# Kernel optimization log

Measured on AMD Instinct MI355X. Metric: run time of the kernel, lower is better.

## Reference

```python
import jax, jax.numpy as jnp
import numpy as np

B, T, H, O = 256, 512, 1024, 256


def setup_inputs() -> dict:
    key = jax.random.key(0)
    k0, k1, k2, k3, k4 = jax.random.split(key, 5)
    scale_ih = 1.0 / np.sqrt(1 + H)
    scale_ho = 1.0 / np.sqrt(H)
    return {
        "x": jax.random.normal(k0, (B, T), dtype=jnp.float32),
        "W_ih": jax.random.normal(k1, (1 + H, H), dtype=jnp.float32) * scale_ih,
        "b_ih": jax.random.normal(k2, (H,), dtype=jnp.float32) * scale_ih,
        "W_ho": jax.random.normal(k3, (H, O), dtype=jnp.float32) * scale_ho,
        "b_ho": jax.random.normal(k4, (O,), dtype=jnp.float32) * scale_ho,
    }


def reference(x, W_ih, b_ih, W_ho, b_ho):
    # Elman RNN cell: hidden = tanh(W_ih @ [x_t; h]); output = W_ho @ h_T.
    # Only the final timestep's output is returned by the original module,
    # so h2o is applied once to the final hidden state (identical math).
    batch = x.shape[0]
    h0 = jnp.zeros((batch, W_ih.shape[1]), dtype=x.dtype)

    def step(h, x_t):  # x_t: [B], h: [B, H]
        combined = jnp.concatenate([x_t[:, None], h], axis=1)  # [B, 1+H]
        h_new = jnp.tanh(combined @ W_ih + b_ih)               # [B, H]
        return h_new, None

    h_final, _ = jax.lax.scan(step, h0, x.T)  # scan over T
    return h_final @ W_ho + b_ho              # [B, O]
```

## Files before the change

kernel.cpp:

```cpp
#include <hip/hip_runtime.h>
#include <hip/hip_bf16.h>


#define Bsz 256
#define Tn  512
#define Hn  1024
#define On  256

typedef __attribute__((ext_vector_type(8))) _Float16 f16x8;
typedef __attribute__((ext_vector_type(4))) float f32x4;
typedef __attribute__((ext_vector_type(4))) int   i32x4;
typedef __attribute__((ext_vector_type(2))) int   i32x2;

__device__ __forceinline__ unsigned f2h(float f) {
    _Float16 h = (_Float16)f;
    union { _Float16 h; unsigned short s; } u; u.h = h;
    return (unsigned)u.s;
}

__device__ __forceinline__ f16x8 as_f16x8(i32x4 v) {
    union { i32x4 i; f16x8 h; } u; u.i = v; return u.h;
}

__device__ __forceinline__ float fast_tanh(float x) {
    float xc = fminf(fmaxf(x, -9.f), 9.f);
    float e  = __builtin_amdgcn_exp2f(xc * 2.8853900817779268f);
    return (e - 1.f) * __builtin_amdgcn_rcpf(e + 1.f);
}

#define MFMA_F16 __builtin_amdgcn_mfma_f32_16x16x32_f16

__device__ __forceinline__ void stage_quarter(const short* __restrict__ hsrc,
                                              short* __restrict__ htile,
                                              int row0, int cg, int kq,
                                              int lane, unsigned tag) {
    const int half = lane >> 5, gl = lane & 31, r0 = cg * 8;
    const short* a0 = hsrc + (size_t)(row0 + r0 + half) * Hn + kq * 256 + gl * 8;
    const short* a1 = a0 + 2 * Hn;
    const short* a2 = a0 + 4 * Hn;
    const short* a3 = a0 + 6 * Hn;
    i32x4 t0, t1, t2, t3;
    for (;;) {
        asm volatile(
            "global_load_dwordx4 %0, %4, off sc0 sc1\n\t"
            "global_load_dwordx4 %1, %5, off sc0 sc1\n\t"
            "global_load_dwordx4 %2, %6, off sc0 sc1\n\t"
            "global_load_dwordx4 %3, %7, off sc0 sc1\n\t"
            "s_waitcnt vmcnt(0)"
            : "=&v"(t0), "=&v"(t1), "=&v"(t2), "=&v"(t3)
            : "v"(a0), "v"(a1), "v"(a2), "v"(a3) : "memory");
        unsigned bad = 0;
#pragma unroll
        for (int e = 0; e < 4; ++e)
            bad |= (unsigned)(t0[e] ^ tag) | (unsigned)(t1[e] ^ tag) |
                   (unsigned)(t2[e] ^ tag) | (unsigned)(t3[e] ^ tag);
        if (!__any(bad & 1u)) break;
        unsigned p0, p3;
        do {
            asm volatile(
                "global_load_dword %0, %2, off sc0 sc1\n\t"
                "global_load_dword %1, %3, off sc0 sc1\n\t"
                "s_waitcnt vmcnt(0)"
                : "=&v"(p0), "=&v"(p3)
                : "v"(a0), "v"(a3) : "memory");
        } while (__any(((p0 ^ tag) | (p3 ^ tag)) & 1u));
    }
    i32x4 tv[4] = {t0, t1, t2, t3};
#pragma unroll
    for (int p = 0; p < 4; ++p) {
        int row = r0 + 2 * p + half;
        int g   = kq * 32 + gl;
        int idx = row * 128 + (g ^ (row & 7));
        *(i32x4*)(htile + idx * 8) = tv[p];
    }
}

__global__ __launch_bounds__(512, 2) void rnn_kernel(
    const float* __restrict__ x,
    const float* __restrict__ W_ih,
    const float* __restrict__ b_ih,
    const float* __restrict__ W_ho,
    const float* __restrict__ b_ho,
    float* __restrict__ out,
    short* __restrict__ hbuf)
{
    const int tid  = threadIdx.x;
    const int lane = tid & 63;
    const int w    = tid >> 6;
    const int cg   = w >> 2;
    const int kq   = w & 3;
    const int q    = lane >> 4;
    const int n    = lane & 15;

    const int i = blockIdx.x & 15;
    const int j = blockIdx.x >> 4;
    const int colbase = j * 128 + cg * 64;
    const int owncol  = colbase + kq * 16 + 4 * q;
    const int row0    = i * 16;

    __shared__ float x_lds[16][Tn + 1];
    __shared__ short htile[16 * Hn];
    __shared__ float redbuf[2][8 * 3 * 256];
    __shared__ int   pairflag[4];

    if (tid < 4) pairflag[tid] = 0;

    for (int idx = tid; idx < 16 * Tn; idx += 512) {
        int r = idx >> 9, tt = idx & (Tn - 1);
        x_lds[r][tt] = x[(row0 + r) * Tn + tt];
    }

    f16x8 wfrag[32];
#pragma unroll
    for (int mt = 0; mt < 4; ++mt)
#pragma unroll
        for (int ks = 0; ks < 8; ++ks) {
#pragma unroll
            for (int e = 0; e < 8; ++e) {
                int k = kq * 256 + ks * 32 + q * 8 + e;
                wfrag[mt * 8 + ks][e] =
                    (_Float16)W_ih[(size_t)(1 + k) * Hn + colbase + mt * 16 + n];
            }
        }
    const float4 bias4 = *(const float4*)(b_ih + owncol);
    const float4 w04   = *(const float4*)(W_ih + owncol);

    __syncthreads();

    short* h0 = hbuf;
    short* h1 = hbuf + Bsz * Hn;
    const int swn   = n & 7;
    const int gbase = kq * 32;
    const int slot  = (q * 16 + n) * 4;
    const f32x4 zero4 = {0.f, 0.f, 0.f, 0.f};

    for (int t = 0; t < Tn; ++t) {
        const float xv = x_lds[n][t];
        f32x4 aown = {bias4.x + xv * w04.x, bias4.y + xv * w04.y,
                      bias4.z + xv * w04.z, bias4.w + xv * w04.w};
        f32x4 hv;

        if (t > 0) {
            stage_quarter((t & 1) ? h1 : h0, htile, row0, cg, kq, lane,
                          (unsigned)((t + 1) >> 1) & 1u);
            asm volatile("s_waitcnt lgkmcnt(0)" ::: "memory");
            if (lane == 0)
                __hip_atomic_fetch_add(&pairflag[kq], 1, __ATOMIC_RELAXED,
                                       __HIP_MEMORY_SCOPE_WORKGROUP);
            while (__hip_atomic_load(&pairflag[kq], __ATOMIC_RELAXED,
                                     __HIP_MEMORY_SCOPE_WORKGROUP) < 2 * t) {}
            asm volatile("" ::: "memory");

            f32x4 acc0 = (kq == 0) ? aown : zero4;
            f32x4 acc1 = (kq == 1) ? aown : zero4;
            f32x4 acc2 = (kq == 2) ? aown : zero4;
            f32x4 acc3 = (kq == 3) ? aown : zero4;
            const i32x4* lrow = (const i32x4*)(htile + n * Hn);
#pragma unroll
            for (int ks = 0; ks < 8; ++ks) {
                f16x8 b = as_f16x8(lrow[(gbase + ks * 4 + q) ^ swn]);
                acc0 = MFMA_F16(wfrag[0 * 8 + ks], b, acc0, 0, 0, 0);
                acc1 = MFMA_F16(wfrag[1 * 8 + ks], b, acc1, 0, 0, 0);
                acc2 = MFMA_F16(wfrag[2 * 8 + ks], b, acc2, 0, 0, 0);
                acc3 = MFMA_F16(wfrag[3 * 8 + ks], b, acc3, 0, 0, 0);
            }

            float* rb = redbuf[t & 1];
#define WRITE_PART(MT, ACC)                                                  \
            if (kq != MT) {                                                  \
                int src = (kq < MT) ? kq : kq - 1;                           \
                *(f32x4*)(rb + ((cg * 4 + MT) * 3 + src) * 256 + slot) = ACC;\
            }
            WRITE_PART(0, acc0)
            WRITE_PART(1, acc1)
            WRITE_PART(2, acc2)
            WRITE_PART(3, acc3)
#undef WRITE_PART
            __syncthreads();

            hv = (kq == 0) ? acc0 : (kq == 1) ? acc1 : (kq == 2) ? acc2 : acc3;
            const float* bp = rb + (cg * 4 + kq) * 3 * 256 + slot;
            f32x4 p0 = *(const f32x4*)(bp);
            f32x4 p1 = *(const f32x4*)(bp + 256);
            f32x4 p2 = *(const f32x4*)(bp + 512);
            hv = hv + p0 + p1 + p2;
        } else {
            hv = aown;
        }

        unsigned tagn = (unsigned)((t + 2) >> 1) & 1u;
        unsigned e0 = f2h(fast_tanh(hv[0])), e1 = f2h(fast_tanh(hv[1]));
        unsigned e2 = f2h(fast_tanh(hv[2])), e3 = f2h(fast_tanh(hv[3]));
        i32x2 pk;
        pk[0] = (int)(((e0 & ~1u) | tagn) | (e1 << 16));
        pk[1] = (int)(((e2 & ~1u) | tagn) | (e3 << 16));
        short* hdst = (((t + 1) & 1) ? h1 : h0) + (size_t)(row0 + n) * Hn + owncol;
        asm volatile("global_store_dwordx2 %0, %1, off sc0 sc1"
                     :: "v"(hdst), "v"(pk) : "memory");
    }

    stage_quarter(h0, htile, row0, cg, kq, lane, 0u);
    __syncthreads();

    f32x4 e0 = zero4, e1 = zero4;
    {
        const i32x4* lrow = (const i32x4*)(htile + n * Hn);
#pragma unroll
        for (int kk = 0; kk < 4; ++kk) {
            f16x8 af = as_f16x8(lrow[(w * 16 + kk * 4 + q) ^ swn]);
            f16x8 b0, b1;
#pragma unroll
            for (int e = 0; e < 8; ++e) {
                const float* wp = W_ho +
                    (size_t)(w * 128 + kk * 32 + q * 8 + e) * On + j * 32 + n;
                b0[e] = (_Float16)wp[0];
                b1[e] = (_Float16)wp[16];
            }
            e0 = MFMA_F16(af, b0, e0, 0, 0, 0);
            e1 = MFMA_F16(af, b1, e1, 0, 0, 0);
        }
    }
    {
        float* re = redbuf[0] + w * 528;
#pragma unroll
        for (int r = 0; r < 4; ++r) {
            re[(4 * q + r) * 33 + n]      = e0[r];
            re[(4 * q + r) * 33 + 16 + n] = e1[r];
        }
    }
    __syncthreads();
    {
        int r = tid >> 5, c = tid & 31;
        float s = b_ho[j * 32 + c];
#pragma unroll
        for (int w8 = 0; w8 < 8; ++w8)
            s += redbuf[0][w8 * 528 + r * 33 + c];
        out[(size_t)(row0 + r) * On + j * 32 + c] = s;
    }
}

extern "C" void kernel_launch(void* const* d_in, const int* in_sizes, int n_in,
                              void* d_out, int out_size, void* d_ws, size_t ws_size,
                              hipStream_t stream) {
    const float* x    = (const float*)d_in[0];
    const float* W_ih = (const float*)d_in[1];
    const float* b_ih = (const float*)d_in[2];
    const float* W_ho = (const float*)d_in[3];
    const float* b_ho = (const float*)d_in[4];
    float* out = (float*)d_out;

    size_t need = (size_t)2 * Bsz * Hn * sizeof(short);
    if (ws_size < need) return;

    short* hbuf = (short*)d_ws;

    rnn_kernel<<<128, 512, 0, stream>>>(x, W_ih, b_ih, W_ho, b_ho, out, hbuf);
}
```

Before: 1.085 ms.

## Give each wave a private h-tile copy, replacing pair flags and block barrier

Each wave now loads the full 16-row slice of its K-quarter of h from global memory into its own private LDS region. Previously two waves each staged half and then synchronised through a pair flag. The block-wide __syncthreads after the partial-sum writes becomes a per-column-group atomic counter barrier among four waves. The aim is to remove inter-wave waits on the serial critical path, at the cost of doubling global/L2 traffic for h staging and more vector registers per wave.

```diff
diff --git a/kernel.cpp b/kernel.cpp
--- a/kernel.cpp
+++ b/kernel.cpp
@@ -30,48 +30,49 @@
 
 #define MFMA_F16 __builtin_amdgcn_mfma_f32_16x16x32_f16
 
-__device__ __forceinline__ void stage_quarter(const short* __restrict__ hsrc,
-                                              short* __restrict__ htile,
-                                              int row0, int cg, int kq,
-                                              int lane, unsigned tag) {
-    const int half = lane >> 5, gl = lane & 31, r0 = cg * 8;
-    const short* a0 = hsrc + (size_t)(row0 + r0 + half) * Hn + kq * 256 + gl * 8;
-    const short* a1 = a0 + 2 * Hn;
-    const short* a2 = a0 + 4 * Hn;
-    const short* a3 = a0 + 6 * Hn;
-    i32x4 t0, t1, t2, t3;
+__device__ __forceinline__ void stage_quarter_priv(
+        const short* __restrict__ hsrc, short* __restrict__ reg_,
+        int row0, int kq, int lane, unsigned tag) {
+    const int half = lane >> 5, gl = lane & 31;
+    const short* a0 = hsrc + (size_t)(row0 + 0  + half) * Hn + kq * 256 + gl * 8;
+    const short* a1 = a0 + 2  * Hn;
+    const short* a2 = a0 + 4  * Hn;
+    const short* a3 = a0 + 6  * Hn;
+    const short* a4 = a0 + 8  * Hn;
+    const short* a5 = a0 + 10 * Hn;
+    const short* a6 = a0 + 12 * Hn;
+    const short* a7 = a0 + 14 * Hn;
+    i32x4 t0, t1, t2, t3, t4, t5, t6, t7;
     for (;;) {
         asm volatile(
-            "global_load_dwordx4 %0, %4, off sc0 sc1\n\t"
-            "global_load_dwordx4 %1, %5, off sc0 sc1\n\t"
-            "global_load_dwordx4 %2, %6, off sc0 sc1\n\t"
-            "global_load_dwordx4 %3, %7, off sc0 sc1\n\t"
+            "global_load_dwordx4 %0, %8, off sc0 sc1\n\t"
+            "global_load_dwordx4 %1, %9, off sc0 sc1\n\t"
+            "global_load_dwordx4 %2, %10, off sc0 sc1\n\t"
+            "global_load_dwordx4 %3, %11, off sc0 sc1\n\t"
+            "global_load_dwordx4 %4, %12, off sc0 sc1\n\t"
+            "global_load_dwordx4 %5, %13, off sc0 sc1\n\t"
+            "global_load_dwordx4 %6, %14, off sc0 sc1\n\t"
+            "global_load_dwordx4 %7, %15, off sc0 sc1\n\t"
             "s_waitcnt vmcnt(0)"
-            : "=&v"(t0), "=&v"(t1), "=&v"(t2), "=&v"(t3)
-            : "v"(a0), "v"(a1), "v"(a2), "v"(a3) : "memory");
+            : "=&v"(t0), "=&v"(t1), "=&v"(t2), "=&v"(t3),
+              "=&v"(t4), "=&v"(t5), "=&v"(t6), "=&v"(t7)
+            : "v"(a0), "v"(a1), "v"(a2), "v"(a3),
+              "v"(a4), "v"(a5), "v"(a6), "v"(a7) : "memory");
         unsigned bad = 0;
 #pragma unroll
         for (int e = 0; e < 4; ++e)
             bad |= (unsigned)(t0[e] ^ tag) | (unsigned)(t1[e] ^ tag) |
-                   (unsigned)(t2[e] ^ tag) | (unsigned)(t3[e] ^ tag);
+                   (unsigned)(t2[e] ^ tag) | (unsigned)(t3[e] ^ tag) |
+                   (unsigned)(t4[e] ^ tag) | (unsigned)(t5[e] ^ tag) |
+                   (unsigned)(t6[e] ^ tag) | (unsigned)(t7[e] ^ tag);
         if (!__any(bad & 1u)) break;
-        unsigned p0, p3;
-        do {
-            asm volatile(
-                "global_load_dword %0, %2, off sc0 sc1\n\t"
-                "global_load_dword %1, %3, off sc0 sc1\n\t"
-                "s_waitcnt vmcnt(0)"
-                : "=&v"(p0), "=&v"(p3)
-                : "v"(a0), "v"(a3) : "memory");
-        } while (__any(((p0 ^ tag) | (p3 ^ tag)) & 1u));
-    }
-    i32x4 tv[4] = {t0, t1, t2, t3};
-#pragma unroll
-    for (int p = 0; p < 4; ++p) {
-        int row = r0 + 2 * p + half;
-        int g   = kq * 32 + gl;
-        int idx = row * 128 + (g ^ (row & 7));
-        *(i32x4*)(htile + idx * 8) = tv[p];
+    }
+    i32x4 tv[8] = {t0, t1, t2, t3, t4, t5, t6, t7};
+#pragma unroll
+    for (int p = 0; p < 8; ++p) {
+        int row = 2 * p + half;
+        int idx = row * 32 + (gl ^ (row & 7));
+        *(i32x4*)(reg_ + idx * 8) = tv[p];
     }
 }
 
@@ -99,11 +100,11 @@
     const int row0    = i * 16;
 
     __shared__ float x_lds[16][Tn + 1];
-    __shared__ short htile[16 * Hn];
+    __shared__ short htile[8 * 16 * 256];
     __shared__ float redbuf[2][8 * 3 * 256];
-    __shared__ int   pairflag[4];
-
-    if (tid < 4) pairflag[tid] = 0;
+    __shared__ int   cgcnt[2];
+
+    if (tid < 2) cgcnt[tid] = 0;
 
     for (int idx = tid; idx < 16 * Tn; idx += 512) {
         int r = idx >> 9, tt = idx & (Tn - 1);
@@ -129,8 +130,7 @@
 
     short* h0 = hbuf;
     short* h1 = hbuf + Bsz * Hn;
-    const int swn   = n & 7;
-    const int gbase = kq * 32;
+    short* myreg = htile + w * 4096;
     const int slot  = (q * 16 + n) * 4;
     const f32x4 zero4 = {0.f, 0.f, 0.f, 0.f};
 
@@ -141,24 +141,18 @@
         f32x4 hv;
 
         if (t > 0) {
-            stage_quarter((t & 1) ? h1 : h0, htile, row0, cg, kq, lane,
-                          (unsigned)((t + 1) >> 1) & 1u);
-            asm volatile("s_waitcnt lgkmcnt(0)" ::: "memory");
-            if (lane == 0)
-                __hip_atomic_fetch_add(&pairflag[kq], 1, __ATOMIC_RELAXED,
-                                       __HIP_MEMORY_SCOPE_WORKGROUP);
-            while (__hip_atomic_load(&pairflag[kq], __ATOMIC_RELAXED,
-                                     __HIP_MEMORY_SCOPE_WORKGROUP) < 2 * t) {}
-            asm volatile("" ::: "memory");
+            stage_quarter_priv((t & 1) ? h1 : h0, myreg, row0, kq, lane,
+                               (unsigned)((t + 1) >> 1) & 1u);
 
             f32x4 acc0 = (kq == 0) ? aown : zero4;
             f32x4 acc1 = (kq == 1) ? aown : zero4;
             f32x4 acc2 = (kq == 2) ? aown : zero4;
             f32x4 acc3 = (kq == 3) ? aown : zero4;
-            const i32x4* lrow = (const i32x4*)(htile + n * Hn);
+            const i32x4* lrow = (const i32x4*)(myreg + n * 256);
+            const int swn = n & 7;
 #pragma unroll
             for (int ks = 0; ks < 8; ++ks) {
-                f16x8 b = as_f16x8(lrow[(gbase + ks * 4 + q) ^ swn]);
+                f16x8 b = as_f16x8(lrow[(ks * 4 + q) ^ swn]);
                 acc0 = MFMA_F16(wfrag[0 * 8 + ks], b, acc0, 0, 0, 0);
                 acc1 = MFMA_F16(wfrag[1 * 8 + ks], b, acc1, 0, 0, 0);
                 acc2 = MFMA_F16(wfrag[2 * 8 + ks], b, acc2, 0, 0, 0);
@@ -176,7 +170,13 @@
             WRITE_PART(2, acc2)
             WRITE_PART(3, acc3)
 #undef WRITE_PART
-            __syncthreads();
+            asm volatile("s_waitcnt lgkmcnt(0)" ::: "memory");
+            if (lane == 0)
+                __hip_atomic_fetch_add(&cgcnt[cg], 1, __ATOMIC_RELAXED,
+                                       __HIP_MEMORY_SCOPE_WORKGROUP);
+            while (__hip_atomic_load(&cgcnt[cg], __ATOMIC_RELAXED,
+                                     __HIP_MEMORY_SCOPE_WORKGROUP) < 4 * t) {}
+            asm volatile("" ::: "memory");
 
             hv = (kq == 0) ? acc0 : (kq == 1) ? acc1 : (kq == 2) ? acc2 : acc3;
             const float* bp = rb + (cg * 4 + kq) * 3 * 256 + slot;
@@ -199,15 +199,47 @@
                      :: "v"(hdst), "v"(pk) : "memory");
     }
 
-    stage_quarter(h0, htile, row0, cg, kq, lane, 0u);
     __syncthreads();
 
+    {
+        const int rs = lane >> 4, g = lane & 15;
+        const short* b0p = h0 + (size_t)(row0 + rs) * Hn + w * 128 + g * 8;
+        const short* b1p = b0p + 4  * Hn;
+        const short* b2p = b0p + 8  * Hn;
+        const short* b3p = b0p + 12 * Hn;
+        i32x4 t0, t1, t2, t3;
+        for (;;) {
+            asm volatile(
+                "global_load_dwordx4 %0, %4, off sc0 sc1\n\t"
+                "global_load_dwordx4 %1, %5, off sc0 sc1\n\t"
+                "global_load_dwordx4 %2, %6, off sc0 sc1\n\t"
+                "global_load_dwordx4 %3, %7, off sc0 sc1\n\t"
+                "s_waitcnt vmcnt(0)"
+                : "=&v"(t0), "=&v"(t1), "=&v"(t2), "=&v"(t3)
+                : "v"(b0p), "v"(b1p), "v"(b2p), "v"(b3p) : "memory");
+            unsigned bad = 0;
+#pragma unroll
+            for (int e = 0; e < 4; ++e)
+                bad |= (unsigned)t0[e] | (unsigned)t1[e] |
+                       (unsigned)t2[e] | (unsigned)t3[e];
+            if (!__any(bad & 1u)) break;
+        }
+        i32x4 tv[4] = {t0, t1, t2, t3};
+#pragma unroll
+        for (int p = 0; p < 4; ++p) {
+            int row = p * 4 + rs;
+            int idx = row * 32 + (g ^ (row & 7));
+            *(i32x4*)(myreg + idx * 8) = tv[p];
+        }
+    }
+
     f32x4 e0 = zero4, e1 = zero4;
     {
-        const i32x4* lrow = (const i32x4*)(htile + n * Hn);
+        const i32x4* lrow = (const i32x4*)(myreg + n * 256);
+        const int swn = n & 7;
 #pragma unroll
         for (int kk = 0; kk < 4; ++kk) {
-            f16x8 af = as_f16x8(lrow[(w * 16 + kk * 4 + q) ^ swn]);
+            f16x8 af = as_f16x8(lrow[(kk * 4 + q) ^ swn]);
             f16x8 b0, b1;
 #pragma unroll
             for (int e = 0; e < 8; ++e) {
```

Measured after the change: 2.841 ms. +161.9%, slower.
